# Optimization experiments

Measured on AMD Instinct MI355X. Metric: run time of the kernel, lower is better.

The kernel has to match this reference:

```python
import jax, jax.numpy as jnp
import numpy as np

N = 50000      # nodes
E2 = 400000    # undirected edges
E = 2 * E2     # directed edges (each undirected edge in both directions)
DIN = 512      # input feature dim
DH = 128       # MLP hidden
C = 8          # num classes / BP channels


def setup_inputs() -> dict:
    key = jax.random.key(0)
    ks = jax.random.split(key, 9)
    x = jax.random.normal(ks[0], (N, DIN), jnp.float32)
    src0 = jax.random.randint(ks[1], (E2,), 0, N)
    dst0 = jax.random.randint(ks[2], (E2,), 0, N)
    # symmetric directed edge list: row 0 = source j, row 1 = target i
    edge_index = jnp.stack([jnp.concatenate([src0, dst0]),
                            jnp.concatenate([dst0, src0])])
    w0 = jax.random.uniform(ks[3], (E2,), jnp.float32, 0.5, 1.5)
    edge_weight = jnp.concatenate([w0, w0])  # reverse edge shares weight
    # edge_rv[e] = index of the reverse of edge e
    edge_rv = jnp.concatenate([jnp.arange(E2) + E2, jnp.arange(E2)])
    W1 = jax.random.normal(ks[4], (DIN, DH), jnp.float32) * 0.05
    b1 = jnp.zeros((DH,), jnp.float32)
    W2 = jax.random.normal(ks[5], (DH, C), jnp.float32) * 0.05
    b2 = jnp.zeros((C,), jnp.float32)
    param = jax.random.normal(ks[6], (C, C), jnp.float32) * 0.1
    return {"x": x, "edge_index": edge_index, "edge_weight": edge_weight,
            "edge_rv": edge_rv, "W1": W1, "b1": b1, "W2": W2, "b2": b2,
            "param": param, "K": 5}


def log_normalize(log_x):
    return log_x - jax.nn.logsumexp(log_x, axis=-1, keepdims=True)


def reference(x, edge_index, edge_weight, edge_rv, W1, b1, W2, b2, param, K):
    # MLP transform + LogSoftmax -> initial log-beliefs [N, C]
    h = jax.nn.relu(x @ W1 + b1)
    log_b0 = jax.nn.log_softmax(h @ W2 + b2, axis=-1)

    # learn_H=True: logH = logsigmoid(param + param^T), [C, C]
    logH = jax.nn.log_sigmoid(param + param.T)
    src, dst = edge_index[0], edge_index[1]
    # per-edge coupling matrix [E, C, C]
    logC = edge_weight[:, None, None] * logH[None, :, :]

    log_b = log_b0
    log_msg = None
    for _ in range(K):
        x_j = log_b[src]                       # gather source beliefs [E, C]
        if log_msg is not None:
            x_j = x_j - log_msg[edge_rv]       # remove reverse message
        # tropical-semiring matvec in log domain: logsumexp over source channel
        log_msg = log_normalize(jax.nn.logsumexp(x_j[:, :, None] + logC, axis=1))
        agg = jax.ops.segment_sum(log_msg, dst, num_segments=N)  # scatter-add
        log_b = log_normalize(log_b0 + agg)
    return log_b
```

## Files before the change

### kernel.cpp

```cpp
#include <hip/hip_runtime.h>
#include <hip/hip_bf16.h>
#include <math.h>

#define NN 50000
#define EE 800000
#define E2K 400000
#define DINK 512
#define DHK 128
#define CK 8
#define KIT 5
#define NBLKS 196
#define NPB 32

typedef __attribute__((ext_vector_type(8))) short short8;
typedef __attribute__((ext_vector_type(4))) float f32x4;

__device__ __forceinline__ unsigned short f2bf(float f) {
    union { float f; unsigned int u; } v;
    v.f = f;
    unsigned int u = v.u;
    unsigned int r = (u + 0x7FFFu + ((u >> 16) & 1u)) >> 16;
    return (unsigned short)r;
}
__device__ __forceinline__ float bfu2f(unsigned int lo16) {
    union { unsigned int u; float f; } v;
    v.u = lo16 << 16;
    return v.f;
}

__global__ __launch_bounds__(256) void prep_kernel(
    const float* __restrict__ W1, const float* __restrict__ param,
    unsigned short* __restrict__ W1t, float* __restrict__ logH) {
    if (blockIdx.x < 256) {
        int idx = blockIdx.x * 256 + threadIdx.x;
        int n = idx >> 9;
        int k = idx & 511;
        W1t[idx] = f2bf(W1[(size_t)k * DHK + n]);
    } else if (threadIdx.x < 64) {
        int t = threadIdx.x;
        int i = t >> 3, j = t & 7;
        float z = param[i * 8 + j] + param[j * 8 + i];
        logH[t] = fminf(z, 0.0f) - log1pf(expf(-fabsf(z)));
    }
}

__global__ __launch_bounds__(256) void mlp_mfma_kernel(
    const float* __restrict__ x, const unsigned short* __restrict__ W1t,
    const float* __restrict__ b1, const float* __restrict__ W2,
    const float* __restrict__ b2, float* __restrict__ logb0) {
    __shared__ unsigned short hs[128 * 136];
    __shared__ float W2s[128 * 8];
    __shared__ float b1s[128];
    __shared__ float b2s[8];

    const int tid = threadIdx.x;
    const int wave = tid >> 6;
    const int lane = tid & 63;
    const int q = lane >> 4;
    const int lm = lane & 15;
    const int wm = wave >> 1, wn = wave & 1;
    const int n0 = blockIdx.x * 128;

    if (tid < 128) b1s[tid] = b1[tid];
    if (tid < 8) b2s[tid] = b2[tid];
    {
        int i = tid * 4;
        *(float4*)&W2s[i] = *(const float4*)&W2[i];
    }
    __syncthreads();

    const float* xptr[4];
#pragma unroll
    for (int mt = 0; mt < 4; ++mt) {
        int r = n0 + wm * 64 + mt * 16 + lm;
        if (r > NN - 1) r = NN - 1;
        xptr[mt] = x + (size_t)r * DINK + q * 8;
    }
    const unsigned short* bptr[4];
#pragma unroll
    for (int nt = 0; nt < 4; ++nt) {
        int c = wn * 64 + nt * 16 + lm;
        bptr[nt] = W1t + (size_t)c * DINK + q * 8;
    }

    f32x4 acc[4][4];
#pragma unroll
    for (int mt = 0; mt < 4; ++mt)
#pragma unroll
        for (int nt = 0; nt < 4; ++nt) acc[mt][nt] = (f32x4){0.f, 0.f, 0.f, 0.f};

    float4 ar[4][2];
    short8 bc[4];
#pragma unroll
    for (int mt = 0; mt < 4; ++mt) {
        ar[mt][0] = *(const float4*)(xptr[mt]);
        ar[mt][1] = *(const float4*)(xptr[mt] + 4);
    }
#pragma unroll
    for (int nt = 0; nt < 4; ++nt) bc[nt] = *(const short8*)(bptr[nt]);

#pragma unroll
    for (int k0 = 32; k0 <= DINK; k0 += 32) {
        float4 ar2[4][2];
        short8 b2f[4];
        if (k0 < DINK) {
#pragma unroll
            for (int mt = 0; mt < 4; ++mt) {
                ar2[mt][0] = *(const float4*)(xptr[mt] + k0);
                ar2[mt][1] = *(const float4*)(xptr[mt] + k0 + 4);
            }
#pragma unroll
            for (int nt = 0; nt < 4; ++nt)
                b2f[nt] = *(const short8*)(bptr[nt] + k0);
        }
        short8 af[4];
#pragma unroll
        for (int mt = 0; mt < 4; ++mt) {
            union { short8 s; __hip_bfloat162 h[4]; } cv;
            cv.h[0] = __float22bfloat162_rn(make_float2(ar[mt][0].x, ar[mt][0].y));
            cv.h[1] = __float22bfloat162_rn(make_float2(ar[mt][0].z, ar[mt][0].w));
            cv.h[2] = __float22bfloat162_rn(make_float2(ar[mt][1].x, ar[mt][1].y));
            cv.h[3] = __float22bfloat162_rn(make_float2(ar[mt][1].z, ar[mt][1].w));
            af[mt] = cv.s;
        }
#pragma unroll
        for (int mt = 0; mt < 4; ++mt)
#pragma unroll
            for (int nt = 0; nt < 4; ++nt)
                acc[mt][nt] = __builtin_amdgcn_mfma_f32_16x16x32_bf16(
                    af[mt], bc[nt], acc[mt][nt], 0, 0, 0);
        if (k0 < DINK) {
#pragma unroll
            for (int mt = 0; mt < 4; ++mt) {
                ar[mt][0] = ar2[mt][0];
                ar[mt][1] = ar2[mt][1];
            }
#pragma unroll
            for (int nt = 0; nt < 4; ++nt) bc[nt] = b2f[nt];
        }
    }

#pragma unroll
    for (int nt = 0; nt < 4; ++nt) {
        int j = wn * 64 + nt * 16 + lm;
        float bj = b1s[j];
#pragma unroll
        for (int mt = 0; mt < 4; ++mt) {
            int rbase = wm * 64 + mt * 16 + q * 4;
#pragma unroll
            for (int r = 0; r < 4; ++r) {
                float h = fmaxf(acc[mt][nt][r] + bj, 0.0f);
                hs[(rbase + r) * 136 + j] = f2bf(h);
            }
        }
    }
    __syncthreads();

    int row = tid >> 1;
    int half = tid & 1;
    const unsigned short* hp = &hs[row * 136 + half * 64];
    float p[8] = {0.f, 0.f, 0.f, 0.f, 0.f, 0.f, 0.f, 0.f};
#pragma unroll
    for (int ch = 0; ch < 8; ++ch) {
        uint4 c4 = *(const uint4*)(hp + ch * 8);
        unsigned int uu[4] = {c4.x, c4.y, c4.z, c4.w};
#pragma unroll
        for (int p2 = 0; p2 < 4; ++p2) {
            float h0 = bfu2f(uu[p2] & 0xFFFFu);
            float h1 = bfu2f(uu[p2] >> 16);
            int j = half * 64 + ch * 8 + p2 * 2;
            const float* w0 = &W2s[j * 8];
            const float* w1 = &W2s[(j + 1) * 8];
#pragma unroll
            for (int c = 0; c < 8; ++c) p[c] = fmaf(h0, w0[c], p[c]);
#pragma unroll
            for (int c = 0; c < 8; ++c) p[c] = fmaf(h1, w1[c], p[c]);
        }
    }
#pragma unroll
    for (int c = 0; c < 8; ++c) p[c] += __shfl_xor(p[c], 1, 64);
    int grow = n0 + row;
    if (half == 0 && grow < NN) {
        float v[8];
        float mx = -1e30f;
#pragma unroll
        for (int c = 0; c < 8; ++c) {
            v[c] = p[c] + b2s[c];
            mx = fmaxf(mx, v[c]);
        }
        float s = 0.0f;
#pragma unroll
        for (int c = 0; c < 8; ++c) s += expf(v[c] - mx);
        float ln = mx + logf(s);
        float4* p0 = (float4*)&logb0[(size_t)grow * 8];
        p0[0] = make_float4(v[0] - ln, v[1] - ln, v[2] - ln, v[3] - ln);
        p0[1] = make_float4(v[4] - ln, v[5] - ln, v[6] - ln, v[7] - ln);
    }
}


__global__ __launch_bounds__(256) void deg_pair_kernel(const int* __restrict__ ei,
                                                       int* __restrict__ cnt) {
    int e = blockIdx.x * 256 + threadIdx.x;
    if (e >= E2K) return;
    int s = ei[e];
    int d = ei[EE + e];
    atomicAdd(&cnt[d], 1);
    atomicAdd(&cnt[s], 1);
}

__global__ __launch_bounds__(256) void scan_partial_kernel(
    const int* __restrict__ cnt, int* __restrict__ partial) {
    __shared__ int sd[256];
    int t = threadIdx.x;
    int i = blockIdx.x * 256 + t;
    sd[t] = (i < NN) ? cnt[i] : 0;
    __syncthreads();
#pragma unroll
    for (int s = 128; s > 0; s >>= 1) {
        if (t < s) sd[t] += sd[t + s];
        __syncthreads();
    }
    if (t == 0) partial[blockIdx.x] = sd[0];
}

__global__ __launch_bounds__(256) void scan_tops_kernel(
    const int* __restrict__ partial, int* __restrict__ tops) {
    __shared__ int sd[256];
    int t = threadIdx.x;
    sd[t] = (t < NBLKS) ? partial[t] : 0;
    __syncthreads();
#pragma unroll
    for (int s = 1; s < 256; s <<= 1) {
        int a = sd[t];
        int b = (t >= s) ? sd[t - s] : 0;
        __syncthreads();
        sd[t] = a + b;
        __syncthreads();
    }
    if (t < NBLKS) tops[t] = (t > 0) ? sd[t - 1] : 0;
}

__global__ __launch_bounds__(256) void scan_write_kernel(
    const int* __restrict__ cnt, const int* __restrict__ tops,
    int* __restrict__ off) {
    __shared__ int sd[256];
    int t = threadIdx.x;
    int i = blockIdx.x * 256 + t;
    int v = (i < NN) ? cnt[i] : 0;
    sd[t] = v;
    __syncthreads();
#pragma unroll
    for (int s = 1; s < 256; s <<= 1) {
        int a = sd[t];
        int b = (t >= s) ? sd[t - s] : 0;
        __syncthreads();
        sd[t] = a + b;
        __syncthreads();
    }
    if (i < NN) off[i] = tops[blockIdx.x] + sd[t] - v;
    if (i == NN - 1) off[NN] = EE;
}

__global__ __launch_bounds__(256) void pos_pair_kernel(
    const int* __restrict__ ei, const float* __restrict__ ew,
    const int* __restrict__ off, int* __restrict__ cnt,
    int2* __restrict__ perm_sw, int* __restrict__ perm_dst,
    int* __restrict__ perm_rvp) {
    int e = blockIdx.x * 256 + threadIdx.x;
    if (e >= E2K) return;
    int s = ei[e];
    int d = ei[EE + e];
    int wbits = __float_as_int(ew[e]);
    int pA = off[d] + atomicAdd(&cnt[d], 1);
    int pB = off[s] + atomicAdd(&cnt[s], 1);
    int2 swA; swA.x = s; swA.y = wbits;
    int2 swB; swB.x = d; swB.y = wbits;
    perm_sw[pA] = swA;
    perm_sw[pB] = swB;
    perm_dst[pA] = d;
    perm_dst[pB] = s;
    perm_rvp[pA] = pB;
    perm_rvp[pB] = pA;
}


__global__ __launch_bounds__(256) void edge_msg_kernel(
    const int2* __restrict__ perm_sw, const float* __restrict__ logH,
    const float* __restrict__ logb0, const float* __restrict__ xin,
    float* __restrict__ msg_out, int first) {
    __shared__ float lH[64];
    if (threadIdx.x < 64) lH[threadIdx.x] = logH[threadIdx.x];
    __syncthreads();
    int p = blockIdx.x * 256 + threadIdx.x;
    if (p >= EE) return;

    int2 sw = perm_sw[p];
    float w = __int_as_float(sw.y);
    const float4* pb = first ? (const float4*)&logb0[(size_t)sw.x * 8]
                             : (const float4*)&xin[(size_t)p * 8];
    float4 v0 = pb[0], v1 = pb[1];
    float xj[8] = {v0.x, v0.y, v0.z, v0.w, v1.x, v1.y, v1.z, v1.w};

    float M = xj[0];
#pragma unroll
    for (int c = 1; c < 8; ++c) M = fmaxf(M, xj[c]);
#pragma unroll
    for (int c = 0; c < 8; ++c) xj[c] -= M;

    float mg[8];
#pragma unroll
    for (int c2 = 0; c2 < 8; ++c2) {
        float ssum = 0.0f;
#pragma unroll
        for (int c1 = 0; c1 < 8; ++c1)
            ssum += __expf(fmaf(w, lH[c1 * 8 + c2], xj[c1]));
        mg[c2] = M + __logf(ssum);
    }

    float4* po = (float4*)&msg_out[(size_t)p * 8];
    po[0] = make_float4(mg[0], mg[1], mg[2], mg[3]);
    po[1] = make_float4(mg[4], mg[5], mg[6], mg[7]);
}

__global__ __launch_bounds__(256) void node_fused_kernel(
    const float* __restrict__ logb0, const int* __restrict__ off,
    const float* __restrict__ msg, const int* __restrict__ perm_dst,
    const int* __restrict__ perm_rvp, float* __restrict__ xin,
    float* __restrict__ out, int last) {
    __shared__ float sb[NPB * 8];
    const int n0 = blockIdx.x * NPB;
    const int t = threadIdx.x;
    const int nl = t >> 3;
    const int c = t & 7;
    const int n = n0 + nl;

    if (n < NN) {
        int j0 = off[n], j1 = off[n + 1];
        float a = logb0[(size_t)n * 8 + c];
        for (int j = j0; j < j1; ++j) a += msg[(size_t)j * 8 + c];
        float mx = a;
#pragma unroll
        for (int s = 1; s < 8; s <<= 1) mx = fmaxf(mx, __shfl_xor(mx, s, 8));
        float sum = __expf(a - mx);
#pragma unroll
        for (int s = 1; s < 8; s <<= 1) sum += __shfl_xor(sum, s, 8);
        float v = a - (mx + __logf(sum));
        if (last) out[(size_t)n * 8 + c] = v;
        sb[nl * 8 + c] = v;
    }
    if (last) return;
    __syncthreads();

    const int nend = (n0 + NPB < NN) ? (n0 + NPB) : NN;
    const int jb0 = off[n0];
    const int jb1 = off[nend];
    const int items = (jb1 - jb0) * 8;
    for (int item = t; item < items; item += 256) {
        int j = jb0 + (item >> 3);
        int c2 = item & 7;
        int dl = perm_dst[j] - n0;
        float val = sb[dl * 8 + c2] - msg[(size_t)j * 8 + c2];
        xin[(size_t)perm_rvp[j] * 8 + c2] = val;
    }
}

extern "C" void kernel_launch(void* const* d_in, const int* in_sizes, int n_in,
                              void* d_out, int out_size, void* d_ws, size_t ws_size,
                              hipStream_t stream) {
    const float* x = (const float*)d_in[0];
    const int* ei = (const int*)d_in[1];
    const float* ew = (const float*)d_in[2];
    const float* W1 = (const float*)d_in[4];
    const float* b1 = (const float*)d_in[5];
    const float* W2 = (const float*)d_in[6];
    const float* b2 = (const float*)d_in[7];
    const float* param = (const float*)d_in[8];
    float* out = (float*)d_out;

    float* wsf = (float*)d_ws;
    float* logH = wsf;
    float* logb0 = logH + 64;
    float* msg = logb0 + (size_t)NN * 8;
    float* xin = msg + (size_t)EE * 8;
    int* off = (int*)(xin + (size_t)EE * 8);
    int2* perm_sw = (int2*)(off + (NN + 1));
    int* perm_rvp = (int*)(perm_sw + EE);
    int* perm_dst = perm_rvp + EE;
    unsigned short* W1t = (unsigned short*)(perm_dst + EE);
    int* cnt = (int*)xin;
    int* partial = cnt + NN;
    int* tops = partial + NBLKS;

    prep_kernel<<<257, 256, 0, stream>>>(W1, param, W1t, logH);
    mlp_mfma_kernel<<<(NN + 127) / 128, 256, 0, stream>>>(x, W1t, b1, W2, b2,
                                                          logb0);

    const int EB = (EE + 255) / 256;
    const int E2B = (E2K + 255) / 256;

    hipMemsetAsync(cnt, 0, (size_t)NN * sizeof(int), stream);
    deg_pair_kernel<<<E2B, 256, 0, stream>>>(ei, cnt);
    scan_partial_kernel<<<NBLKS, 256, 0, stream>>>(cnt, partial);
    scan_tops_kernel<<<1, 256, 0, stream>>>(partial, tops);
    scan_write_kernel<<<NBLKS, 256, 0, stream>>>(cnt, tops, off);
    hipMemsetAsync(cnt, 0, (size_t)NN * sizeof(int), stream);
    pos_pair_kernel<<<E2B, 256, 0, stream>>>(ei, ew, off, cnt, perm_sw,
                                             perm_dst, perm_rvp);

    const int NB = (NN + NPB - 1) / NPB;
    for (int it = 0; it < KIT; ++it) {
        int first = (it == 0) ? 1 : 0;
        int last = (it == KIT - 1) ? 1 : 0;
        edge_msg_kernel<<<EB, 256, 0, stream>>>(perm_sw, logH, logb0, xin, msg,
                                                first);
        node_fused_kernel<<<NB, 256, 0, stream>>>(logb0, off, msg, perm_dst,
                                                  perm_rvp, xin, out, last);
    }
}
```

Measured before the change: 481.2 us.

## Store per-edge messages and cavity inputs in fp16 and normalize messages

```diff
diff --git a/kernel.cpp b/kernel.cpp
--- a/kernel.cpp
+++ b/kernel.cpp
@@ -1,5 +1,6 @@
 #include <hip/hip_runtime.h>
 #include <hip/hip_bf16.h>
+#include <hip/hip_fp16.h>
 #include <math.h>
 
 #define NN 50000
@@ -265,19 +266,19 @@
 __global__ __launch_bounds__(256) void pos_pair_kernel(
     const int* __restrict__ ei, const float* __restrict__ ew,
     const int* __restrict__ off, int* __restrict__ cnt,
-    int2* __restrict__ perm_sw, int* __restrict__ perm_dst,
-    int* __restrict__ perm_rvp) {
+    int* __restrict__ perm_src, float* __restrict__ perm_w,
+    int* __restrict__ perm_dst, int* __restrict__ perm_rvp) {
     int e = blockIdx.x * 256 + threadIdx.x;
     if (e >= E2K) return;
     int s = ei[e];
     int d = ei[EE + e];
-    int wbits = __float_as_int(ew[e]);
+    float w = ew[e];
     int pA = off[d] + atomicAdd(&cnt[d], 1);
     int pB = off[s] + atomicAdd(&cnt[s], 1);
-    int2 swA; swA.x = s; swA.y = wbits;
-    int2 swB; swB.x = d; swB.y = wbits;
-    perm_sw[pA] = swA;
-    perm_sw[pB] = swB;
+    perm_src[pA] = s;
+    perm_src[pB] = d;
+    perm_w[pA] = w;
+    perm_w[pB] = w;
     perm_dst[pA] = d;
     perm_dst[pB] = s;
     perm_rvp[pA] = pB;
@@ -286,21 +287,29 @@
 
 
 __global__ __launch_bounds__(256) void edge_msg_kernel(
-    const int2* __restrict__ perm_sw, const float* __restrict__ logH,
-    const float* __restrict__ logb0, const float* __restrict__ xin,
-    float* __restrict__ msg_out, int first) {
+    const int* __restrict__ perm_src, const float* __restrict__ perm_w,
+    const float* __restrict__ logH, const float* __restrict__ logb0,
+    const uint4* __restrict__ xin16, uint4* __restrict__ msg16, int first) {
     __shared__ float lH[64];
     if (threadIdx.x < 64) lH[threadIdx.x] = logH[threadIdx.x];
     __syncthreads();
     int p = blockIdx.x * 256 + threadIdx.x;
     if (p >= EE) return;
 
-    int2 sw = perm_sw[p];
-    float w = __int_as_float(sw.y);
-    const float4* pb = first ? (const float4*)&logb0[(size_t)sw.x * 8]
-                             : (const float4*)&xin[(size_t)p * 8];
-    float4 v0 = pb[0], v1 = pb[1];
-    float xj[8] = {v0.x, v0.y, v0.z, v0.w, v1.x, v1.y, v1.z, v1.w};
+    float w = perm_w[p];
+    float xj[8];
+    if (first) {
+        int s = perm_src[p];
+        const float4* pb = (const float4*)&logb0[(size_t)s * 8];
+        float4 v0 = pb[0], v1 = pb[1];
+        xj[0] = v0.x; xj[1] = v0.y; xj[2] = v0.z; xj[3] = v0.w;
+        xj[4] = v1.x; xj[5] = v1.y; xj[6] = v1.z; xj[7] = v1.w;
+    } else {
+        union { uint4 u; _Float16 h[8]; } cv;
+        cv.u = xin16[p];
+#pragma unroll
+        for (int c = 0; c < 8; ++c) xj[c] = (float)cv.h[c];
+    }
 
     float M = xj[0];
 #pragma unroll
@@ -315,18 +324,26 @@
 #pragma unroll
         for (int c1 = 0; c1 < 8; ++c1)
             ssum += __expf(fmaf(w, lH[c1 * 8 + c2], xj[c1]));
-        mg[c2] = M + __logf(ssum);
-    }
-
-    float4* po = (float4*)&msg_out[(size_t)p * 8];
-    po[0] = make_float4(mg[0], mg[1], mg[2], mg[3]);
-    po[1] = make_float4(mg[4], mg[5], mg[6], mg[7]);
+        mg[c2] = __logf(ssum);
+    }
+    float mm = mg[0];
+#pragma unroll
+    for (int c = 1; c < 8; ++c) mm = fmaxf(mm, mg[c]);
+    float se = 0.0f;
+#pragma unroll
+    for (int c = 0; c < 8; ++c) se += __expf(mg[c] - mm);
+    float ln = mm + __logf(se);
+
+    union { uint4 u; _Float16 h[8]; } ov;
+#pragma unroll
+    for (int c = 0; c < 8; ++c) ov.h[c] = (_Float16)(mg[c] - ln);
+    msg16[p] = ov.u;
 }
 
 __global__ __launch_bounds__(256) void node_fused_kernel(
     const float* __restrict__ logb0, const int* __restrict__ off,
-    const float* __restrict__ msg, const int* __restrict__ perm_dst,
-    const int* __restrict__ perm_rvp, float* __restrict__ xin,
+    const uint4* __restrict__ msg16, const int* __restrict__ perm_dst,
+    const int* __restrict__ perm_rvp, uint4* __restrict__ xin16,
     float* __restrict__ out, int last) {
     __shared__ float sb[NPB * 8];
     const int n0 = blockIdx.x * NPB;
@@ -334,11 +351,12 @@
     const int nl = t >> 3;
     const int c = t & 7;
     const int n = n0 + nl;
+    const _Float16* msgh = (const _Float16*)msg16;
 
     if (n < NN) {
         int j0 = off[n], j1 = off[n + 1];
         float a = logb0[(size_t)n * 8 + c];
-        for (int j = j0; j < j1; ++j) a += msg[(size_t)j * 8 + c];
+        for (int j = j0; j < j1; ++j) a += (float)msgh[(size_t)j * 8 + c];
         float mx = a;
 #pragma unroll
         for (int s = 1; s < 8; s <<= 1) mx = fmaxf(mx, __shfl_xor(mx, s, 8));
@@ -352,6 +370,7 @@
     if (last) return;
     __syncthreads();
 
+    _Float16* xinh = (_Float16*)xin16;
     const int nend = (n0 + NPB < NN) ? (n0 + NPB) : NN;
     const int jb0 = off[n0];
     const int jb1 = off[nend];
@@ -360,8 +379,8 @@
         int j = jb0 + (item >> 3);
         int c2 = item & 7;
         int dl = perm_dst[j] - n0;
-        float val = sb[dl * 8 + c2] - msg[(size_t)j * 8 + c2];
-        xin[(size_t)perm_rvp[j] * 8 + c2] = val;
+        float val = sb[dl * 8 + c2] - (float)msgh[(size_t)j * 8 + c2];
+        xinh[(size_t)perm_rvp[j] * 8 + c2] = (_Float16)val;
     }
 }
 
@@ -381,14 +400,15 @@
     float* wsf = (float*)d_ws;
     float* logH = wsf;
     float* logb0 = logH + 64;
-    float* msg = logb0 + (size_t)NN * 8;
-    float* xin = msg + (size_t)EE * 8;
-    int* off = (int*)(xin + (size_t)EE * 8);
-    int2* perm_sw = (int2*)(off + (NN + 1));
-    int* perm_rvp = (int*)(perm_sw + EE);
+    uint4* msg16 = (uint4*)(logb0 + (size_t)NN * 8);
+    uint4* xin16 = msg16 + EE;
+    int* off = (int*)(xin16 + EE);
+    int* perm_src = off + (NN + 1);
+    float* perm_w = (float*)(perm_src + EE);
+    int* perm_rvp = (int*)(perm_w + EE);
     int* perm_dst = perm_rvp + EE;
     unsigned short* W1t = (unsigned short*)(perm_dst + EE);
-    int* cnt = (int*)xin;
+    int* cnt = (int*)xin16;
     int* partial = cnt + NN;
     int* tops = partial + NBLKS;
 
@@ -405,16 +425,16 @@
     scan_tops_kernel<<<1, 256, 0, stream>>>(partial, tops);
     scan_write_kernel<<<NBLKS, 256, 0, stream>>>(cnt, tops, off);
     hipMemsetAsync(cnt, 0, (size_t)NN * sizeof(int), stream);
-    pos_pair_kernel<<<E2B, 256, 0, stream>>>(ei, ew, off, cnt, perm_sw,
-                                             perm_dst, perm_rvp);
+    pos_pair_kernel<<<E2B, 256, 0, stream>>>(ei, ew, off, cnt, perm_src,
+                                             perm_w, perm_dst, perm_rvp);
 
     const int NB = (NN + NPB - 1) / NPB;
     for (int it = 0; it < KIT; ++it) {
         int first = (it == 0) ? 1 : 0;
         int last = (it == KIT - 1) ? 1 : 0;
-        edge_msg_kernel<<<EB, 256, 0, stream>>>(perm_sw, logH, logb0, xin, msg,
-                                                first);
-        node_fused_kernel<<<NB, 256, 0, stream>>>(logb0, off, msg, perm_dst,
-                                                  perm_rvp, xin, out, last);
-    }
-}
+        edge_msg_kernel<<<EB, 256, 0, stream>>>(perm_src, perm_w, logH, logb0,
+                                                xin16, msg16, first);
+        node_fused_kernel<<<NB, 256, 0, stream>>>(logb0, off, msg16, perm_dst,
+                                                  perm_rvp, xin16, out, last);
+    }
+}
```

Result: no change. 479.5 us (-0.4%).
